# Kernel optimization log

Hardware: AMD Instinct MI355X
Metric: run time of the kernel (lower is better)

Reference implementation:

```python
import jax, jax.numpy as jnp
import numpy as np

T, D = 4096, 1024
S = 32768
DIST_DIM = 20
BINS = jnp.array([1, 2, 3, 4, 8, 16, 32, 64], dtype=jnp.int64)


def setup_inputs() -> dict:
    key = jax.random.key(0)
    ks = jax.random.split(key, 16)
    scale = 1.0 / np.sqrt(D)
    inp = {
        "embeds": jax.random.normal(ks[0], (T, D), dtype=jnp.float32),
        "states": jax.random.normal(ks[1], (T, D), dtype=jnp.float32),
        # MHA (1 head) projection params, torch Linear convention: x @ W.T + b
        "Wq": jax.random.normal(ks[2], (D, D), dtype=jnp.float32) * scale,
        "bq": jnp.zeros((D,), dtype=jnp.float32),
        "Wk": jax.random.normal(ks[3], (D, D), dtype=jnp.float32) * scale,
        "bk": jnp.zeros((D,), dtype=jnp.float32),
        "Wv": jax.random.normal(ks[4], (D, D), dtype=jnp.float32) * scale,
        "bv": jnp.zeros((D,), dtype=jnp.float32),
        "Wo": jax.random.normal(ks[5], (D, D), dtype=jnp.float32) * scale,
        "bo": jnp.zeros((D,), dtype=jnp.float32),
        # distance embedding table: len(bins)+1 = 9 rows
        "dist_embed": jax.random.normal(ks[6], (9, DIST_DIM), dtype=jnp.float32),
        "span_starts": jax.random.randint(ks[7], (S,), 0, T - 30, dtype=jnp.int64),
        "span_lengths": jax.random.randint(ks[8], (S,), 0, 30, dtype=jnp.int64),
    }
    return inp


def reference(embeds, states, Wq, bq, Wk, bk, Wv, bv, Wo, bo, dist_embed,
              span_starts, span_lengths):
    d = states.shape[1]
    # Single-head attention: query=states, key=states, value=embeds (seq len T, batch 1)
    q = states @ Wq.T + bq                      # [T, D]
    k = states @ Wk.T + bk                      # [T, D]
    v = embeds @ Wv.T + bv                      # [T, D]
    scores = (q @ k.T) / jnp.sqrt(jnp.asarray(d, q.dtype))   # [T, T]
    attn = jax.nn.softmax(scores, axis=-1)
    attn_embeds = (attn @ v) @ Wo.T + bo        # [T, D]

    ends = span_starts + span_lengths           # inclusive end, width 1..30
    # ragged per-span segment sum over [start, end] via prefix sums
    cs = jnp.concatenate([jnp.zeros((1, d), attn_embeds.dtype),
                          jnp.cumsum(attn_embeds, axis=0)], axis=0)  # [T+1, D]
    span_sum = cs[ends + 1] - cs[span_starts]   # [S, D]

    span_start_end = jnp.concatenate([states[span_starts], states[ends]], axis=1)  # [S, 2D]

    lengths = span_lengths + 1                  # len(span) = end - start + 1
    bin_idx = jnp.sum(lengths[:, None] > BINS[None, :], axis=-1)  # [S] in [0, 8]
    len_embed = dist_embed[bin_idx]             # [S, DIST_DIM] (dropout omitted: eval mode)

    return jnp.concatenate([span_sum, span_start_end, len_embed], axis=1)  # [S, 3D+20]
```

## Files before the change

### kernel.cpp

```cpp
#include <hip/hip_runtime.h>
#include <hip/hip_bf16.h>


typedef __attribute__((ext_vector_type(8))) short bf16x8;
typedef __attribute__((ext_vector_type(4))) float f32x4;

#define T_DIM 4096
#define D_DIM 1024
#define S_NUM 32768
#define LDS_STRIDE 40

__global__ __launch_bounds__(256) void cast_bf16(const float* __restrict__ s,
                                                 __hip_bfloat16* __restrict__ d) {
  int i = blockIdx.x * 256 + threadIdx.x;
  float2 v = ((const float2*)s)[i];
  __hip_bfloat162 o;
  o.x = __float2bfloat16(v.x);
  o.y = __float2bfloat16(v.y);
  ((__hip_bfloat162*)d)[i] = o;
}

enum { OUT_F32 = 0, OUT_BF16 = 1, OUT_BF16_T = 2 };

template <int MODE, bool HAS_BIAS>
__global__ __launch_bounds__(256) void gemm_nt(const __hip_bfloat16* __restrict__ A,
                                               const __hip_bfloat16* __restrict__ B,
                                               const float* __restrict__ bias,
                                               void* __restrict__ Cv,
                                               int M, int N, int K, float alpha) {
  __shared__ __hip_bfloat16 As[64 * LDS_STRIDE];
  __shared__ __hip_bfloat16 Bs[64 * LDS_STRIDE];
  const int tid = threadIdx.x;
  const int wave = tid >> 6;
  const int lane = tid & 63;
  const int bm = blockIdx.y * 64;
  const int bn = blockIdx.x * 64;
  const int sr = tid >> 2;
  const int sc = (tid & 3) * 8;
  const __hip_bfloat16* Ag = A + (size_t)(bm + sr) * K + sc;
  const __hip_bfloat16* Bg = B + (size_t)(bn + sr) * K + sc;
  const int wtr = (wave >> 1) * 32;
  const int wtc = (wave & 1) * 32;
  const int lr = lane & 15;
  const int lk = (lane >> 4) * 8;
  f32x4 acc[2][2] = {};

  for (int k0 = 0; k0 < K; k0 += 32) {
    __syncthreads();
    *(bf16x8*)&As[sr * LDS_STRIDE + sc] = *(const bf16x8*)(Ag + k0);
    *(bf16x8*)&Bs[sr * LDS_STRIDE + sc] = *(const bf16x8*)(Bg + k0);
    __syncthreads();
    bf16x8 a0 = *(const bf16x8*)&As[(wtr + lr) * LDS_STRIDE + lk];
    bf16x8 a1 = *(const bf16x8*)&As[(wtr + 16 + lr) * LDS_STRIDE + lk];
    bf16x8 b0 = *(const bf16x8*)&Bs[(wtc + lr) * LDS_STRIDE + lk];
    bf16x8 b1 = *(const bf16x8*)&Bs[(wtc + 16 + lr) * LDS_STRIDE + lk];
    acc[0][0] = __builtin_amdgcn_mfma_f32_16x16x32_bf16(a0, b0, acc[0][0], 0, 0, 0);
    acc[0][1] = __builtin_amdgcn_mfma_f32_16x16x32_bf16(a0, b1, acc[0][1], 0, 0, 0);
    acc[1][0] = __builtin_amdgcn_mfma_f32_16x16x32_bf16(a1, b0, acc[1][0], 0, 0, 0);
    acc[1][1] = __builtin_amdgcn_mfma_f32_16x16x32_bf16(a1, b1, acc[1][1], 0, 0, 0);
  }

#pragma unroll
  for (int i = 0; i < 2; i++) {
#pragma unroll
    for (int j = 0; j < 2; j++) {
      const int col = bn + wtc + j * 16 + lr;
      const float bb = HAS_BIAS ? bias[col] : 0.0f;
#pragma unroll
      for (int r = 0; r < 4; r++) {
        const int row = bm + wtr + i * 16 + (lane >> 4) * 4 + r;
        const float val = acc[i][j][r] * alpha + bb;
        if (MODE == OUT_F32)
          ((float*)Cv)[(size_t)row * N + col] = val;
        else if (MODE == OUT_BF16)
          ((__hip_bfloat16*)Cv)[(size_t)row * N + col] = __float2bfloat16(val);
        else
          ((__hip_bfloat16*)Cv)[(size_t)col * M + row] = __float2bfloat16(val);
      }
    }
  }
}

__global__ __launch_bounds__(256) void softmax_row(const float* __restrict__ Sc,
                                                   __hip_bfloat16* __restrict__ P) {
  const int row = blockIdx.x;
  const int tid = threadIdx.x;
  const int lane = tid & 63, wave = tid >> 6;
  const float2* sr = (const float2*)(Sc + (size_t)row * T_DIM);
  __hip_bfloat162* pr = (__hip_bfloat162*)(P + (size_t)row * T_DIM);
  float2 v[8];
  float mx = -3.0e38f;
#pragma unroll
  for (int i = 0; i < 8; i++) {
    v[i] = sr[tid + i * 256];
    mx = fmaxf(mx, fmaxf(v[i].x, v[i].y));
  }
#pragma unroll
  for (int o = 1; o < 64; o <<= 1) mx = fmaxf(mx, __shfl_xor(mx, o));
  __shared__ float red[8];
  if (lane == 0) red[wave] = mx;
  __syncthreads();
  mx = fmaxf(fmaxf(red[0], red[1]), fmaxf(red[2], red[3]));
  float sum = 0.0f;
#pragma unroll
  for (int i = 0; i < 8; i++) {
    v[i].x = __expf(v[i].x - mx);
    v[i].y = __expf(v[i].y - mx);
    sum += v[i].x + v[i].y;
  }
#pragma unroll
  for (int o = 1; o < 64; o <<= 1) sum += __shfl_xor(sum, o);
  if (lane == 0) red[4 + wave] = sum;
  __syncthreads();
  const float inv = 1.0f / (red[4] + red[5] + red[6] + red[7]);
#pragma unroll
  for (int i = 0; i < 8; i++) {
    __hip_bfloat162 o2;
    o2.x = __float2bfloat16(v[i].x * inv);
    o2.y = __float2bfloat16(v[i].y * inv);
    pr[tid + i * 256] = o2;
  }
}

__global__ __launch_bounds__(256) void colsum_chunks(const float* __restrict__ x,
                                                     float* __restrict__ part) {
  const int col = blockIdx.x * 256 + threadIdx.x;
  const int ch = blockIdx.y;
  const float* p = x + (size_t)ch * 64 * D_DIM + col;
  float s = 0.0f;
#pragma unroll 8
  for (int i = 0; i < 64; i++) s += p[i * D_DIM];
  part[ch * D_DIM + col] = s;
}

__global__ __launch_bounds__(256) void scan_chunks(float* part) {
  const int col = blockIdx.x * 256 + threadIdx.x;
  float run = 0.0f;
  for (int ch = 0; ch < 64; ch++) {
    const float t = part[ch * D_DIM + col];
    part[ch * D_DIM + col] = run;
    run += t;
  }
}

__global__ __launch_bounds__(256) void write_cs(const float* __restrict__ x,
                                                const float* __restrict__ part,
                                                float* __restrict__ cs) {
  const int col = blockIdx.x * 256 + threadIdx.x;
  const int ch = blockIdx.y;
  float run = part[ch * D_DIM + col];
  if (ch == 0) cs[col] = 0.0f;
  const float* p = x + (size_t)ch * 64 * D_DIM + col;
  float* q = cs + ((size_t)(ch * 64 + 1)) * D_DIM + col;
  for (int i = 0; i < 64; i++) {
    run += p[i * D_DIM];
    q[i * D_DIM] = run;
  }
}

__global__ __launch_bounds__(256) void span_gather(const float* __restrict__ cs,
                                                   const float* __restrict__ states,
                                                   const float* __restrict__ dist,
                                                   const int* __restrict__ starts,
                                                   const int* __restrict__ lens,
                                                   float* __restrict__ out) {
  const int s = blockIdx.x;
  const int start = starts[s];
  const int len = lens[s];
  const int end = start + len;
  const int length = len + 1;
  const int bin = (length > 1) + (length > 2) + (length > 3) + (length > 4) +
                  (length > 8) + (length > 16) + (length > 32) + (length > 64);
  const float4* csS = (const float4*)(cs + (size_t)start * D_DIM);
  const float4* csE = (const float4*)(cs + (size_t)(end + 1) * D_DIM);
  const float4* stS = (const float4*)(states + (size_t)start * D_DIM);
  const float4* stE = (const float4*)(states + (size_t)end * D_DIM);
  const float4* de = (const float4*)(dist + bin * 20);
  float4* o = (float4*)(out + (size_t)s * 3092);
  for (int j = threadIdx.x; j < 773; j += 256) {
    float4 r;
    if (j < 256) {
      float4 a = csE[j], b = csS[j];
      r = make_float4(a.x - b.x, a.y - b.y, a.z - b.z, a.w - b.w);
    } else if (j < 512) {
      r = stS[j - 256];
    } else if (j < 768) {
      r = stE[j - 512];
    } else {
      r = de[j - 768];
    }
    o[j] = r;
  }
}

extern "C" void kernel_launch(void* const* d_in, const int* in_sizes, int n_in,
                              void* d_out, int out_size, void* d_ws, size_t ws_size,
                              hipStream_t stream) {
  const float* embeds = (const float*)d_in[0];
  const float* states = (const float*)d_in[1];
  const float* Wq = (const float*)d_in[2];
  const float* bq = (const float*)d_in[3];
  const float* Wk = (const float*)d_in[4];
  const float* bk = (const float*)d_in[5];
  const float* Wv = (const float*)d_in[6];
  const float* bv = (const float*)d_in[7];
  const float* Wo = (const float*)d_in[8];
  const float* bo = (const float*)d_in[9];
  const float* dist = (const float*)d_in[10];
  const int* starts = (const int*)d_in[11];
  const int* lens = (const int*)d_in[12];
  float* out = (float*)d_out;

  const size_t TD = (size_t)T_DIM * D_DIM;
  const size_t DD = (size_t)D_DIM * D_DIM;
  const size_t TT = (size_t)T_DIM * T_DIM;

  char* w = (char*)d_ws;
  size_t off = 0;
  auto alloc = [&](size_t bytes) {
    char* p = w + off;
    off = (off + bytes + 255) & ~(size_t)255;
    return p;
  };
  __hip_bfloat16* states_bf = (__hip_bfloat16*)alloc(TD * 2);
  __hip_bfloat16* embeds_bf = (__hip_bfloat16*)alloc(TD * 2);
  __hip_bfloat16* Wq_bf = (__hip_bfloat16*)alloc(DD * 2);
  __hip_bfloat16* Wk_bf = (__hip_bfloat16*)alloc(DD * 2);
  __hip_bfloat16* Wv_bf = (__hip_bfloat16*)alloc(DD * 2);
  __hip_bfloat16* Wo_bf = (__hip_bfloat16*)alloc(DD * 2);
  __hip_bfloat16* q_bf = (__hip_bfloat16*)alloc(TD * 2);
  __hip_bfloat16* k_bf = (__hip_bfloat16*)alloc(TD * 2);
  __hip_bfloat16* vT_bf = (__hip_bfloat16*)alloc(TD * 2);
  __hip_bfloat16* ae_bf = (__hip_bfloat16*)alloc(TD * 2);
  float* scores = (float*)alloc(TT * 4);
  __hip_bfloat16* attn_bf = (__hip_bfloat16*)alloc(TT * 2);
  float* ao = (float*)alloc(TD * 4);
  float* cs = (float*)alloc((size_t)(T_DIM + 1) * D_DIM * 4);
  float* part = (float*)alloc(64 * D_DIM * 4);
  if (off > ws_size) return;

  cast_bf16<<<TD / 512, 256, 0, stream>>>(states, states_bf);
  cast_bf16<<<TD / 512, 256, 0, stream>>>(embeds, embeds_bf);
  cast_bf16<<<DD / 512, 256, 0, stream>>>(Wq, Wq_bf);
  cast_bf16<<<DD / 512, 256, 0, stream>>>(Wk, Wk_bf);
  cast_bf16<<<DD / 512, 256, 0, stream>>>(Wv, Wv_bf);
  cast_bf16<<<DD / 512, 256, 0, stream>>>(Wo, Wo_bf);

  dim3 gProj(D_DIM / 64, T_DIM / 64);
  gemm_nt<OUT_BF16, true><<<gProj, 256, 0, stream>>>(states_bf, Wq_bf, bq, q_bf,
                                                     T_DIM, D_DIM, D_DIM, 1.0f);
  gemm_nt<OUT_BF16, true><<<gProj, 256, 0, stream>>>(states_bf, Wk_bf, bk, k_bf,
                                                     T_DIM, D_DIM, D_DIM, 1.0f);
  gemm_nt<OUT_BF16_T, true><<<gProj, 256, 0, stream>>>(embeds_bf, Wv_bf, bv, vT_bf,
                                                       T_DIM, D_DIM, D_DIM, 1.0f);

  dim3 gScore(T_DIM / 64, T_DIM / 64);
  gemm_nt<OUT_F32, false><<<gScore, 256, 0, stream>>>(q_bf, k_bf, nullptr, scores,
                                                      T_DIM, T_DIM, D_DIM, 0.03125f);

  softmax_row<<<T_DIM, 256, 0, stream>>>(scores, attn_bf);

  gemm_nt<OUT_BF16, false><<<gProj, 256, 0, stream>>>(attn_bf, vT_bf, nullptr, ae_bf,
                                                      T_DIM, D_DIM, T_DIM, 1.0f);
  gemm_nt<OUT_F32, true><<<gProj, 256, 0, stream>>>(ae_bf, Wo_bf, bo, ao,
                                                    T_DIM, D_DIM, D_DIM, 1.0f);

  colsum_chunks<<<dim3(4, 64), 256, 0, stream>>>(ao, part);
  scan_chunks<<<4, 256, 0, stream>>>(part);
  write_cs<<<dim3(4, 64), 256, 0, stream>>>(ao, part, cs);

  span_gather<<<S_NUM, 256, 0, stream>>>(cs, states, dist, starts, lens, out);
}
```

Measured before the change: 809.0 us.

## Enlarge GEMM tiles to 128x128 and load tiles via global_load_lds

Replaces the 64x64 GEMM with a 128x128 tile kernel where each wave computes a 64x64 sub-tile (4x4 MFMA accumulators), raising operand reuse per LDS read. Tiles are now staged straight from global memory into LDS with the global_load_lds builtin instead of going through registers, and the padded LDS stride is dropped. All six GEMM launches switch to the new kernel with halved grid dimensions. The unpadded layout may cause LDS bank conflicts, and the projection GEMMs now launch only 256 blocks, which may underfill the GPU.

```diff
diff --git a/kernel.cpp b/kernel.cpp
--- a/kernel.cpp
+++ b/kernel.cpp
@@ -8,7 +8,11 @@
 #define T_DIM 4096
 #define D_DIM 1024
 #define S_NUM 32768
-#define LDS_STRIDE 40
+
+#define GLOBAL_LOAD_LDS16(gptr, ldsptr)                                        \
+  __builtin_amdgcn_global_load_lds(                                            \
+      (const __attribute__((address_space(1))) void*)(gptr),                   \
+      (__attribute__((address_space(3))) void*)(ldsptr), 16, 0, 0)
 
 __global__ __launch_bounds__(256) void cast_bf16(const float* __restrict__ s,
                                                  __hip_bfloat16* __restrict__ d) {
@@ -23,49 +27,64 @@
 enum { OUT_F32 = 0, OUT_BF16 = 1, OUT_BF16_T = 2 };
 
 template <int MODE, bool HAS_BIAS>
-__global__ __launch_bounds__(256) void gemm_nt(const __hip_bfloat16* __restrict__ A,
-                                               const __hip_bfloat16* __restrict__ B,
-                                               const float* __restrict__ bias,
-                                               void* __restrict__ Cv,
-                                               int M, int N, int K, float alpha) {
-  __shared__ __hip_bfloat16 As[64 * LDS_STRIDE];
-  __shared__ __hip_bfloat16 Bs[64 * LDS_STRIDE];
+__global__ __launch_bounds__(256) void gemm_nt128(const __hip_bfloat16* __restrict__ A,
+                                                  const __hip_bfloat16* __restrict__ B,
+                                                  const float* __restrict__ bias,
+                                                  void* __restrict__ Cv,
+                                                  int M, int N, int K, float alpha) {
+  __shared__ __hip_bfloat16 As[128 * 32];
+  __shared__ __hip_bfloat16 Bs[128 * 32];
   const int tid = threadIdx.x;
   const int wave = tid >> 6;
   const int lane = tid & 63;
-  const int bm = blockIdx.y * 64;
-  const int bn = blockIdx.x * 64;
-  const int sr = tid >> 2;
-  const int sc = (tid & 3) * 8;
-  const __hip_bfloat16* Ag = A + (size_t)(bm + sr) * K + sc;
-  const __hip_bfloat16* Bg = B + (size_t)(bn + sr) * K + sc;
-  const int wtr = (wave >> 1) * 32;
-  const int wtc = (wave & 1) * 32;
+  const int bm = blockIdx.y * 128;
+  const int bn = blockIdx.x * 128;
+
+  const int srow = (lane >> 2);
+  const int scol = (lane & 3) * 8;
+  const __hip_bfloat16* Ag0 = A + (size_t)(bm + wave * 16 + srow) * K + scol;
+  const __hip_bfloat16* Ag1 = A + (size_t)(bm + 64 + wave * 16 + srow) * K + scol;
+  const __hip_bfloat16* Bg0 = B + (size_t)(bn + wave * 16 + srow) * K + scol;
+  const __hip_bfloat16* Bg1 = B + (size_t)(bn + 64 + wave * 16 + srow) * K + scol;
+  __hip_bfloat16* lAs0 = As + wave * 512;
+  __hip_bfloat16* lAs1 = As + (4 + wave) * 512;
+  __hip_bfloat16* lBs0 = Bs + wave * 512;
+  __hip_bfloat16* lBs1 = Bs + (4 + wave) * 512;
+
+  const int wtr = (wave >> 1) * 64;
+  const int wtc = (wave & 1) * 64;
   const int lr = lane & 15;
   const int lk = (lane >> 4) * 8;
-  f32x4 acc[2][2] = {};
+  f32x4 acc[4][4] = {};
 
   for (int k0 = 0; k0 < K; k0 += 32) {
     __syncthreads();
-    *(bf16x8*)&As[sr * LDS_STRIDE + sc] = *(const bf16x8*)(Ag + k0);
-    *(bf16x8*)&Bs[sr * LDS_STRIDE + sc] = *(const bf16x8*)(Bg + k0);
+    GLOBAL_LOAD_LDS16(Ag0 + k0, lAs0);
+    GLOBAL_LOAD_LDS16(Ag1 + k0, lAs1);
+    GLOBAL_LOAD_LDS16(Bg0 + k0, lBs0);
+    GLOBAL_LOAD_LDS16(Bg1 + k0, lBs1);
     __syncthreads();
-    bf16x8 a0 = *(const bf16x8*)&As[(wtr + lr) * LDS_STRIDE + lk];
-    bf16x8 a1 = *(const bf16x8*)&As[(wtr + 16 + lr) * LDS_STRIDE + lk];
-    bf16x8 b0 = *(const bf16x8*)&Bs[(wtc + lr) * LDS_STRIDE + lk];
-    bf16x8 b1 = *(const bf16x8*)&Bs[(wtc + 16 + lr) * LDS_STRIDE + lk];
-    acc[0][0] = __builtin_amdgcn_mfma_f32_16x16x32_bf16(a0, b0, acc[0][0], 0, 0, 0);
-    acc[0][1] = __builtin_amdgcn_mfma_f32_16x16x32_bf16(a0, b1, acc[0][1], 0, 0, 0);
-    acc[1][0] = __builtin_amdgcn_mfma_f32_16x16x32_bf16(a1, b0, acc[1][0], 0, 0, 0);
-    acc[1][1] = __builtin_amdgcn_mfma_f32_16x16x32_bf16(a1, b1, acc[1][1], 0, 0, 0);
-  }
-
-#pragma unroll
-  for (int i = 0; i < 2; i++) {
-#pragma unroll
-    for (int j = 0; j < 2; j++) {
-      const int col = bn + wtc + j * 16 + lr;
-      const float bb = HAS_BIAS ? bias[col] : 0.0f;
+
+    bf16x8 a[4], b[4];
+#pragma unroll
+    for (int i = 0; i < 4; i++)
+      a[i] = *(const bf16x8*)&As[(wtr + i * 16 + lr) * 32 + lk];
+#pragma unroll
+    for (int j = 0; j < 4; j++)
+      b[j] = *(const bf16x8*)&Bs[(wtc + j * 16 + lr) * 32 + lk];
+#pragma unroll
+    for (int i = 0; i < 4; i++)
+#pragma unroll
+      for (int j = 0; j < 4; j++)
+        acc[i][j] = __builtin_amdgcn_mfma_f32_16x16x32_bf16(a[i], b[j], acc[i][j], 0, 0, 0);
+  }
+
+#pragma unroll
+  for (int j = 0; j < 4; j++) {
+    const int col = bn + wtc + j * 16 + lr;
+    const float bb = HAS_BIAS ? bias[col] : 0.0f;
+#pragma unroll
+    for (int i = 0; i < 4; i++) {
 #pragma unroll
       for (int r = 0; r < 4; r++) {
         const int row = bm + wtr + i * 16 + (lane >> 4) * 4 + r;
@@ -246,24 +265,24 @@
   cast_bf16<<<DD / 512, 256, 0, stream>>>(Wv, Wv_bf);
   cast_bf16<<<DD / 512, 256, 0, stream>>>(Wo, Wo_bf);
 
-  dim3 gProj(D_DIM / 64, T_DIM / 64);
-  gemm_nt<OUT_BF16, true><<<gProj, 256, 0, stream>>>(states_bf, Wq_bf, bq, q_bf,
-                                                     T_DIM, D_DIM, D_DIM, 1.0f);
-  gemm_nt<OUT_BF16, true><<<gProj, 256, 0, stream>>>(states_bf, Wk_bf, bk, k_bf,
-                                                     T_DIM, D_DIM, D_DIM, 1.0f);
-  gemm_nt<OUT_BF16_T, true><<<gProj, 256, 0, stream>>>(embeds_bf, Wv_bf, bv, vT_bf,
+  dim3 gProj(D_DIM / 128, T_DIM / 128);
+  gemm_nt128<OUT_BF16, true><<<gProj, 256, 0, stream>>>(states_bf, Wq_bf, bq, q_bf,
+                                                        T_DIM, D_DIM, D_DIM, 1.0f);
+  gemm_nt128<OUT_BF16, true><<<gProj, 256, 0, stream>>>(states_bf, Wk_bf, bk, k_bf,
+                                                        T_DIM, D_DIM, D_DIM, 1.0f);
+  gemm_nt128<OUT_BF16_T, true><<<gProj, 256, 0, stream>>>(embeds_bf, Wv_bf, bv, vT_bf,
+                                                          T_DIM, D_DIM, D_DIM, 1.0f);
+
+  dim3 gScore(T_DIM / 128, T_DIM / 128);
+  gemm_nt128<OUT_F32, false><<<gScore, 256, 0, stream>>>(q_bf, k_bf, nullptr, scores,
+                                                         T_DIM, T_DIM, D_DIM, 0.03125f);
+
+  softmax_row<<<T_DIM, 256, 0, stream>>>(scores, attn_bf);
+
+  gemm_nt128<OUT_BF16, false><<<gProj, 256, 0, stream>>>(attn_bf, vT_bf, nullptr, ae_bf,
+                                                         T_DIM, D_DIM, T_DIM, 1.0f);
+  gemm_nt128<OUT_F32, true><<<gProj, 256, 0, stream>>>(ae_bf, Wo_bf, bo, ao,
                                                        T_DIM, D_DIM, D_DIM, 1.0f);
-
-  dim3 gScore(T_DIM / 64, T_DIM / 64);
-  gemm_nt<OUT_F32, false><<<gScore, 256, 0, stream>>>(q_bf, k_bf, nullptr, scores,
-                                                      T_DIM, T_DIM, D_DIM, 0.03125f);
-
-  softmax_row<<<T_DIM, 256, 0, stream>>>(scores, attn_bf);
-
-  gemm_nt<OUT_BF16, false><<<gProj, 256, 0, stream>>>(attn_bf, vT_bf, nullptr, ae_bf,
-                                                      T_DIM, D_DIM, T_DIM, 1.0f);
-  gemm_nt<OUT_F32, true><<<gProj, 256, 0, stream>>>(ae_bf, Wo_bf, bo, ao,
-                                                    T_DIM, D_DIM, D_DIM, 1.0f);
 
   colsum_chunks<<<dim3(4, 64), 256, 0, stream>>>(ao, part);
   scan_chunks<<<4, 256, 0, stream>>>(part);
```

Result: no change. 801.9 us (-0.9%).
